# Performance work log

Hardware: AMD Instinct MI355X
Metric: run time of the kernel (lower is better)

## Reference

```python
import jax, jax.numpy as jnp
import numpy as np

N = 20000   # nodes (spots)
E = 100000  # edges (kNN spatial graph, avg degree 5)
IN = 256    # input feature dim = out_dim[-1]
D = 512     # per-head output dim = in_dim (gene count)
H = 4       # heads
NEG_SLOPE = 0.2  # DGL GATv2Conv default negative_slope; fc LeakyReLU slope is also 0.2


def setup_inputs() -> dict:
    key = jax.random.key(0)
    ks = jax.random.split(key, 10)
    s = 0.02
    return {
        "z": jax.random.normal(ks[0], (N, IN), jnp.float32),
        "src": jax.random.randint(ks[1], (E,), 0, N, jnp.int32),
        "dst": jax.random.randint(ks[2], (E,), 0, N, jnp.int32),
        "W_src": jax.random.normal(ks[3], (IN, H * D), jnp.float32) * s,
        "b_src": jnp.zeros((H * D,), jnp.float32),
        "W_dst": jax.random.normal(ks[4], (IN, H * D), jnp.float32) * s,
        "b_dst": jnp.zeros((H * D,), jnp.float32),
        "attn": jax.random.normal(ks[5], (H, D), jnp.float32) * s,
        "gat_bias": jnp.zeros((H * D,), jnp.float32),
        "W_fc": jax.random.normal(ks[6], (H * D, D), jnp.float32) * s,
        "b_fc": jnp.zeros((D,), jnp.float32),
    }


def reference(z, src, dst, W_src, b_src, W_dst, b_dst, attn, gat_bias, W_fc, b_fc):
    # GATv2Conv (DGL semantics, share_weights=False, eval mode so dropout is identity)
    feat_src = (z @ W_src + b_src).reshape(N, H, D)  # [N,H,D]
    feat_dst = (z @ W_dst + b_dst).reshape(N, H, D)  # [N,H,D]
    # per-edge GATv2 score: a^T LeakyReLU(Wsrc h_u + Wdst h_v)
    e = jax.nn.leaky_relu(feat_src[src] + feat_dst[dst], NEG_SLOPE)  # [E,H,D]
    score = jnp.einsum('ehd,hd->eh', e, attn)                        # [E,H]
    # edge softmax over incoming edges of each dst node (numerically stable)
    m = jax.lax.stop_gradient(
        jnp.full((N, H), -jnp.inf, score.dtype).at[dst].max(score))
    ex = jnp.exp(score - m[dst])                                     # [E,H]
    denom = jnp.zeros((N, H), ex.dtype).at[dst].add(ex)              # [N,H]
    alpha = ex / denom[dst]                                          # [E,H]
    # scatter-aggregate messages
    msg = alpha[:, :, None] * feat_src[src]                          # [E,H,D]
    rst = jnp.zeros((N, H, D), msg.dtype).at[dst].add(msg)
    rst = rst + gat_bias.reshape(1, H, D)
    # flatten heads, then fused Linear + LeakyReLU(0.2)
    flat = rst.reshape(N, H * D)
    return jax.nn.leaky_relu(flat @ W_fc + b_fc, NEG_SLOPE)          # [N,D]
```

## Files before the change

kernel.cpp:

```cpp
#include <hip/hip_runtime.h>
#include <hip/hip_bf16.h>
#include <math.h>

#define H_HEADS 4
#define D_HEAD 512
#define HD 2048
#define IN_DIM 256
#define OUTD 512
#define NEG 0.2f

typedef __hip_bfloat16 bf16;
typedef _Float16 f16;
typedef __attribute__((ext_vector_type(2))) _Float16 h2v;
typedef __attribute__((ext_vector_type(8))) short s16x8;
typedef __attribute__((ext_vector_type(4))) float f32x4;

__device__ __forceinline__ float bflo(unsigned w) { union { unsigned u; float f; } x; x.u = w << 16; return x.f; }
__device__ __forceinline__ float bfhi(unsigned w) { union { unsigned u; float f; } x; x.u = w & 0xffff0000u; return x.f; }

template<int MODE>
__global__ __launch_bounds__(256)
void mfma_gemm_kernel(const bf16* __restrict__ A, int lda, long aOff,
                      const bf16* __restrict__ Bt, int ldb, long bOff,
                      const float* __restrict__ bias, long biasOff,
                      const float* __restrict__ bias2, const int* __restrict__ rowptr,
                      void* __restrict__ Cv, int ldc, long cOff,
                      int M, int K)
{
    constexpr int SMEM_BYTES = (MODE == 1) ? (64 * 132 * 4) : (128 * 136 * 2);
    static_assert(SMEM_BYTES >= 4 * 4096 * 2, "staging dbuf must fit");
    __shared__ __align__(16) char smem_raw[SMEM_BYTES];
    bf16* stg = (bf16*)smem_raw;

    const int tid  = threadIdx.x;
    const int r0   = blockIdx.y * 128;
    const int n0   = blockIdx.x * 128;
    const int z    = blockIdx.z;
    const int lane = tid & 63;
    const int wave = tid >> 6;
    const int wr   = (wave >> 1) * 64;
    const int wc   = (wave & 1) * 64;
    const int l15  = lane & 15;
    const int quad = lane >> 4;

    const bf16* Az = A + aOff * (long)z;
    const bf16* Bz = Bt + bOff * (long)z;

    f32x4 acc[4][4];
    #pragma unroll
    for (int i = 0; i < 4; i++)
        #pragma unroll
        for (int j = 0; j < 4; j++)
            #pragma unroll
            for (int r = 0; r < 4; r++) acc[i][j][r] = 0.f;

    const int srow = tid >> 2;
    const int skof = (((tid & 3) ^ ((srow >> 1) & 3)) * 8);
    const int swz  = (l15 >> 1) & 3;

    auto stage_tile = [&](int c, int k0) {
        bf16* As = stg + c * 8192;
        bf16* Bs = As + 4096;
        #pragma unroll
        for (int p = 0; p < 2; p++) {
            int ar = r0 + p * 64 + srow;
            if (ar >= M) ar = M - 1;
            const bf16* ga = Az + (size_t)ar * lda + k0 + skof;
            __builtin_amdgcn_global_load_lds(
                (const __attribute__((address_space(1))) void*)ga,
                (__attribute__((address_space(3))) void*)(As + (p * 256 + tid) * 8),
                16, 0, 0);
            const bf16* gb = Bz + (size_t)(n0 + p * 64 + srow) * ldb + k0 + skof;
            __builtin_amdgcn_global_load_lds(
                (const __attribute__((address_space(1))) void*)gb,
                (__attribute__((address_space(3))) void*)(Bs + (p * 256 + tid) * 8),
                16, 0, 0);
        }
    };

    stage_tile(0, 0);
    int cbuf = 0;
    for (int k0 = 0; k0 < K; k0 += 32) {
        __syncthreads();
        if (k0 + 32 < K) stage_tile(cbuf ^ 1, k0 + 32);

        const bf16* As = stg + cbuf * 8192;
        const bf16* Bs = As + 4096;
        s16x8 af[4], bg[4];
        #pragma unroll
        for (int i = 0; i < 4; i++)
            af[i] = *(const s16x8*)(As + (wr + i * 16 + l15) * 32 + (quad ^ swz) * 8);
        #pragma unroll
        for (int j = 0; j < 4; j++)
            bg[j] = *(const s16x8*)(Bs + (wc + j * 16 + l15) * 32 + (quad ^ swz) * 8);
        #pragma unroll
        for (int i = 0; i < 4; i++)
            #pragma unroll
            for (int j = 0; j < 4; j++)
                acc[i][j] = __builtin_amdgcn_mfma_f32_16x16x32_bf16(af[i], bg[j], acc[i][j], 0, 0, 0);
        cbuf ^= 1;
    }
    __syncthreads();

    if (MODE == 0 || MODE == 2) {
        float bv[4];
        #pragma unroll
        for (int j = 0; j < 4; j++)
            bv[j] = bias ? bias[biasOff * (long)z + n0 + wc + j * 16 + l15] : 0.f;

        const long cb = cOff * (long)z;

        if (MODE == 0) {
            bf16* Cs = (bf16*)smem_raw;
            #pragma unroll
            for (int i = 0; i < 4; i++)
                #pragma unroll
                for (int j = 0; j < 4; j++)
                    #pragma unroll
                    for (int r = 0; r < 4; r++)
                        Cs[(wr + i * 16 + quad * 4 + r) * 136 + wc + j * 16 + l15] =
                            __float2bfloat16(acc[i][j][r] + bv[j]);
        } else {
            f16* Cs = (f16*)smem_raw;
            #pragma unroll
            for (int i = 0; i < 4; i++)
                #pragma unroll
                for (int j = 0; j < 4; j++)
                    #pragma unroll
                    for (int r = 0; r < 4; r++)
                        Cs[(wr + i * 16 + quad * 4 + r) * 136 + wc + j * 16 + l15] =
                            (f16)(acc[i][j][r] + bv[j]);
        }
        __syncthreads();
        #pragma unroll
        for (int it = 0; it < 8; it++) {
            const int idx  = it * 256 + tid;
            const int lrow = idx >> 4;
            const int lcol = (idx & 15) * 8;
            const int grow = r0 + lrow;
            if (grow < M)
                *(uint4*)((short*)Cv + cb + (size_t)grow * ldc + n0 + lcol) =
                    *(const uint4*)((const short*)smem_raw + lrow * 136 + lcol);
        }
    } else {
        float* C = (float*)Cv;
        float* Csf = (float*)smem_raw;

        #pragma unroll
        for (int p = 0; p < 2; p++) {
            __syncthreads();
            if (wr == p * 64) {
                #pragma unroll
                for (int i = 0; i < 4; i++)
                    #pragma unroll
                    for (int j = 0; j < 4; j++)
                        #pragma unroll
                        for (int r = 0; r < 4; r++)
                            Csf[(i * 16 + quad * 4 + r) * 132 + wc + j * 16 + l15] = acc[i][j][r];
            }
            __syncthreads();
            #pragma unroll
            for (int it = 0; it < 8; it++) {
                const int idx  = it * 256 + tid;
                const int lrow = idx >> 5;
                const int lcol = (idx & 31) * 4;
                const int grow = r0 + p * 64 + lrow;
                if (grow < M) {
                    const int gcol = n0 + lcol;
                    float4 v  = *(const float4*)(Csf + lrow * 132 + lcol);
                    const float4 c4 = *(const float4*)(bias + gcol);
                    const float4 b4 = *(const float4*)(bias2 + gcol);
                    const bool has = rowptr[grow + 1] > rowptr[grow];
                    v.x += c4.x + (has ? b4.x : 0.f);
                    v.y += c4.y + (has ? b4.y : 0.f);
                    v.z += c4.z + (has ? b4.z : 0.f);
                    v.w += c4.w + (has ? b4.w : 0.f);
                    v.x = v.x > 0.f ? v.x : NEG * v.x;
                    v.y = v.y > 0.f ? v.y : NEG * v.y;
                    v.z = v.z > 0.f ? v.z : NEG * v.z;
                    v.w = v.w > 0.f ? v.w : NEG * v.w;
                    *(float4*)(C + (size_t)grow * ldc + gcol) = v;
                }
            }
        }
    }
}

__global__ __launch_bounds__(256)
void prep_kernel(const float* __restrict__ W_src, const float* __restrict__ W_dst,
                 const float* __restrict__ W_fc, const float* __restrict__ b_src,
                 const float* __restrict__ b_dst, const float* __restrict__ attn,
                 const float* __restrict__ b_fc, const float* __restrict__ gat_bias,
                 bf16* __restrict__ WsbT, bf16* __restrict__ WdbT,
                 bf16* __restrict__ WfcT, bf16* __restrict__ Wsb,
                 float* __restrict__ bias_cat, f16* __restrict__ atn16,
                 int* __restrict__ cnt, int nCnt,
                 float* __restrict__ cvec, float* __restrict__ bsW_tot, int prepBlocks)
{
    __shared__ float red[256];
    if ((int)blockIdx.x >= prepBlocks) {
        const int b = blockIdx.x - prepBlocks;
        const int t = threadIdx.x;
        const bool isCvec = b < OUTD;
        const int j = isCvec ? b : b - OUTD;
        const float* vec = isCvec ? gat_bias : b_src;
        float s = 0.f;
        for (int k = t; k < HD; k += 256)
            s = fmaf(vec[k], W_fc[(size_t)k * OUTD + j], s);
        red[t] = s;
        __syncthreads();
        for (int o = 128; o > 0; o >>= 1) {
            if (t < o) red[t] += red[t + o];
            __syncthreads();
        }
        if (t == 0) {
            if (isCvec) cvec[j] = red[0] + b_fc[j];
            else bsW_tot[j] = red[0];
        }
        return;
    }
    int idx = blockIdx.x * 256 + threadIdx.x;
    if (idx < 524288) {
        const int n = idx >> 8, k = idx & 255;
        WsbT[idx] = __float2bfloat16(W_src[(size_t)k * HD + n]);
        return;
    }
    idx -= 524288;
    if (idx < 524288) {
        const int n = idx >> 8, k = idx & 255;
        WdbT[idx] = __float2bfloat16(W_dst[(size_t)k * HD + n]);
        return;
    }
    idx -= 524288;
    if (idx < 1048576) {
        const int n = idx >> 9, t = idx & 511;
        const int h = n >> 9, j = n & 511;
        WfcT[idx] = __float2bfloat16(W_fc[(size_t)(h * 512 + t) * OUTD + j]);
        return;
    }
    idx -= 1048576;
    if (idx < 524288) {
        Wsb[idx] = __float2bfloat16(W_src[idx]);
        return;
    }
    idx -= 524288;
    if (idx < 2 * HD) {
        bias_cat[idx] = (idx < HD) ? b_src[idx] : b_dst[idx - HD];
        return;
    }
    idx -= 2 * HD;
    if (idx < HD) {
        atn16[idx] = (f16)attn[idx];
        return;
    }
    idx -= HD;
    if (idx < nCnt) cnt[idx] = 0;
}

__global__ void cast_hist_kernel(const float* __restrict__ S, bf16* __restrict__ T,
                                 long n4, const int* __restrict__ dst,
                                 int* __restrict__ cnt, int E)
{
    long t = (long)blockIdx.x * 256 + threadIdx.x;
    if (t < n4) {
        const long i = t * 4;
        const float4 v = *(const float4*)(S + i);
        T[i + 0] = __float2bfloat16(v.x);
        T[i + 1] = __float2bfloat16(v.y);
        T[i + 2] = __float2bfloat16(v.z);
        T[i + 3] = __float2bfloat16(v.w);
        return;
    }
    t -= n4;
    if (t < E) atomicAdd(&cnt[dst[t]], 1);
}

__global__ __launch_bounds__(1024)
void scan_kernel(const int* __restrict__ cnt, int* __restrict__ rowptr,
                 int* __restrict__ cursor, int n)
{
    __shared__ int wsum[16];
    __shared__ int carry_s;
    const int tid  = threadIdx.x;
    const int lane = tid & 63;
    const int wv   = tid >> 6;
    if (tid == 0) { carry_s = 0; rowptr[0] = 0; cursor[0] = 0; }
    __syncthreads();
    for (int base = 0; base < n; base += 1024) {
        const int i = base + tid;
        int v = (i < n) ? cnt[i] : 0;
        #pragma unroll
        for (int d = 1; d < 64; d <<= 1) {
            const int t = __shfl_up(v, d, 64);
            if (lane >= d) v += t;
        }
        if (lane == 63) wsum[wv] = v;
        __syncthreads();
        if (tid < 16) {
            int w = wsum[tid];
            #pragma unroll
            for (int d = 1; d < 16; d <<= 1) {
                const int t = __shfl_up(w, d, 64);
                if (tid >= d) w += t;
            }
            wsum[tid] = w;
        }
        __syncthreads();
        const int incl = v + (wv ? wsum[wv - 1] : 0) + carry_s;
        if (i < n) {
            rowptr[i + 1] = incl;
            if (i + 1 < n) cursor[i + 1] = incl;
        }
        __syncthreads();
        if (tid == 1023) carry_s += wsum[15];
        __syncthreads();
    }
}

__global__ void scatter_kernel(const int* __restrict__ src, const int* __restrict__ dst,
                               int* __restrict__ cursor, int* __restrict__ csr_src, int E)
{
    const int e = blockIdx.x * 256 + threadIdx.x;
    if (e >= E) return;
    const int pos = atomicAdd(&cursor[dst[e]], 1);
    csr_src[pos] = src[e];
}

__device__ __forceinline__ float score_head_h2(const uint4 pa, const uint4 pb, const uint4 at)
{
    const unsigned* ua = (const unsigned*)&pa;
    const unsigned* ub = (const unsigned*)&pb;
    const unsigned* ut = (const unsigned*)&at;
    h2v acc = (h2v)(_Float16)0.f;
    const h2v c06 = (h2v)(_Float16)0.6f;
    const h2v c04 = (h2v)(_Float16)0.4f;
    #pragma unroll
    for (int c = 0; c < 4; c++) {
        union { unsigned u; h2v h; } A, B, T, S, Ab;
        A.u = ua[c]; B.u = ub[c]; T.u = ut[c];
        S.h = A.h + B.h;
        Ab.u = S.u & 0x7fff7fffu;
        const h2v l = S.h * c06 + Ab.h * c04;
        acc += l * T.h;
    }
    return (float)acc.x + (float)acc.y;
}

__global__ __launch_bounds__(256)
void score_agg_kernel(const f16* __restrict__ fs, const f16* __restrict__ fd,
                      const bf16* __restrict__ zb,
                      const int* __restrict__ rowptr, const int* __restrict__ csr_src,
                      const f16* __restrict__ atn16, bf16* __restrict__ agg, int N)
{
    const int h    = threadIdx.x >> 6;
    const int lane = threadIdx.x & 63;
    const int v    = blockIdx.x;
    if (v >= N) return;

    const uint4 at = *(const uint4*)(atn16 + h * D_HEAD + lane * 8);
    const f16* fsh = fs + h * D_HEAD + (size_t)lane * 8;

    const int off0 = rowptr[v], off1 = rowptr[v + 1];
    const int deg  = off1 - off0;
    float acc[4] = {0.f, 0.f, 0.f, 0.f};
    float den = 0.f;

    const uint4 fdr = *(const uint4*)(fd + (size_t)v * HD + h * D_HEAD + lane * 8);

    for (int e = 0; e < deg; e += 4) {
        const int i0 = off0 + e;
        const int i1 = off0 + ((e + 1 < deg) ? e + 1 : e);
        const int i2 = off0 + ((e + 2 < deg) ? e + 2 : e);
        const int i3 = off0 + ((e + 3 < deg) ? e + 3 : e);
        const int u0 = csr_src[i0], u1 = csr_src[i1], u2 = csr_src[i2], u3 = csr_src[i3];

        const uint4 pa0 = *(const uint4*)(fsh + (size_t)u0 * HD);
        const uint4 pa1 = *(const uint4*)(fsh + (size_t)u1 * HD);
        const uint4 pa2 = *(const uint4*)(fsh + (size_t)u2 * HD);
        const uint4 pa3 = *(const uint4*)(fsh + (size_t)u3 * HD);
        const uint2 z0 = *(const uint2*)(zb + (size_t)u0 * IN_DIM + lane * 4);
        const uint2 z1 = *(const uint2*)(zb + (size_t)u1 * IN_DIM + lane * 4);
        const uint2 z2 = *(const uint2*)(zb + (size_t)u2 * IN_DIM + lane * 4);
        const uint2 z3 = *(const uint2*)(zb + (size_t)u3 * IN_DIM + lane * 4);

        float s0 = score_head_h2(pa0, fdr, at);
        float s1 = score_head_h2(pa1, fdr, at);
        float s2 = score_head_h2(pa2, fdr, at);
        float s3 = score_head_h2(pa3, fdr, at);
        #pragma unroll
        for (int ofs = 32; ofs > 0; ofs >>= 1) {
            s0 += __shfl_xor(s0, ofs, 64);
            s1 += __shfl_xor(s1, ofs, 64);
            s2 += __shfl_xor(s2, ofs, 64);
            s3 += __shfl_xor(s3, ofs, 64);
        }
        const float e0 = __expf(s0);
        const float e1 = (e + 1 < deg) ? __expf(s1) : 0.f;
        const float e2 = (e + 2 < deg) ? __expf(s2) : 0.f;
        const float e3 = (e + 3 < deg) ? __expf(s3) : 0.f;
        den += e0 + e1 + e2 + e3;
        const float zc0[4] = {bflo(z0.x), bfhi(z0.x), bflo(z0.y), bfhi(z0.y)};
        const float zc1[4] = {bflo(z1.x), bfhi(z1.x), bflo(z1.y), bfhi(z1.y)};
        const float zc2[4] = {bflo(z2.x), bfhi(z2.x), bflo(z2.y), bfhi(z2.y)};
        const float zc3[4] = {bflo(z3.x), bfhi(z3.x), bflo(z3.y), bfhi(z3.y)};
        #pragma unroll
        for (int c = 0; c < 4; c++)
            acc[c] += (e0 * zc0[c] + e1 * zc1[c]) + (e2 * zc2[c] + e3 * zc3[c]);
    }
    if (deg > 0) {
        const float inv = 1.f / den;
        #pragma unroll
        for (int c = 0; c < 4; c++) acc[c] *= inv;
    }

    union { uint2 u; short s[4]; } pk;
    #pragma unroll
    for (int c = 0; c < 4; c++) {
        const bf16 b = __float2bfloat16(acc[c]);
        pk.s[c] = *(const short*)&b;
    }
    *(uint2*)(agg + (size_t)v * (H_HEADS * IN_DIM) + h * IN_DIM + lane * 4) = pk.u;
}

__global__ __launch_bounds__(256)
void score_csr_kernel(const f16* __restrict__ fs, const f16* __restrict__ fd,
                      const int* __restrict__ rowptr, const int* __restrict__ csr_src,
                      const f16* __restrict__ atn16, float* __restrict__ expbuf,
                      float* __restrict__ denomB, int N)
{
    const int wave = threadIdx.x >> 6;
    const int lane = threadIdx.x & 63;
    const int wgid = blockIdx.x * 4 + wave;
    const int nw   = gridDim.x * 4;

    uint4 at[H_HEADS];
    #pragma unroll
    for (int h = 0; h < H_HEADS; h++)
        at[h] = *(const uint4*)(atn16 + h * D_HEAD + lane * 8);

    for (int v = wgid; v < N; v += nw) {
        const int off0 = rowptr[v], off1 = rowptr[v + 1];
        if (off0 == off1) continue;
        uint4 fdr[H_HEADS];
        #pragma unroll
        for (int h = 0; h < H_HEADS; h++)
            fdr[h] = *(const uint4*)(fd + (size_t)v * HD + h * D_HEAD + lane * 8);

        float4 den = make_float4(0.f, 0.f, 0.f, 0.f);
        for (int o = off0; o < off1; o += 2) {
            const bool two = (o + 1 < off1);
            const int u0 = csr_src[o];
            const int u1 = two ? csr_src[o + 1] : u0;
            const f16* f0 = fs + (size_t)u0 * HD + lane * 8;
            const f16* f1 = fs + (size_t)u1 * HD + lane * 8;
            uint4 pa0[H_HEADS], pa1[H_HEADS];
            #pragma unroll
            for (int h = 0; h < H_HEADS; h++) pa0[h] = *(const uint4*)(f0 + h * D_HEAD);
            #pragma unroll
            for (int h = 0; h < H_HEADS; h++) pa1[h] = *(const uint4*)(f1 + h * D_HEAD);

            float s0[H_HEADS], s1[H_HEADS];
            #pragma unroll
            for (int h = 0; h < H_HEADS; h++) {
                s0[h] = score_head_h2(pa0[h], fdr[h], at[h]);
                s1[h] = score_head_h2(pa1[h], fdr[h], at[h]);
            }
            #pragma unroll
            for (int ofs = 32; ofs > 0; ofs >>= 1) {
                #pragma unroll
                for (int h = 0; h < H_HEADS; h++) {
                    s0[h] += __shfl_xor(s0[h], ofs, 64);
                    s1[h] += __shfl_xor(s1[h], ofs, 64);
                }
            }
            const float4 e0 = make_float4(expf(s0[0]), expf(s0[1]), expf(s0[2]), expf(s0[3]));
            den.x += e0.x; den.y += e0.y; den.z += e0.z; den.w += e0.w;
            float4 e1;
            if (two) {
                e1 = make_float4(expf(s1[0]), expf(s1[1]), expf(s1[2]), expf(s1[3]));
                den.x += e1.x; den.y += e1.y; den.z += e1.z; den.w += e1.w;
            }
            if (lane == 0) {
                *(float4*)(expbuf + (size_t)o * H_HEADS) = e0;
                if (two) *(float4*)(expbuf + (size_t)(o + 1) * H_HEADS) = e1;
            }
        }
        if (lane == 0) *(float4*)(denomB + (size_t)v * H_HEADS) = den;
    }
}

__global__ __launch_bounds__(256)
void agg_z_kernel(const bf16* __restrict__ zb, const int* __restrict__ rowptr,
                  const int* __restrict__ csr_src, const float* __restrict__ expbuf,
                  const float* __restrict__ denomB, bf16* __restrict__ agg, int N)
{
    const int wave = threadIdx.x >> 6;
    const int lane = threadIdx.x & 63;
    const int wgid = blockIdx.x * 4 + wave;
    const int nw   = gridDim.x * 4;

    for (int v = wgid; v < N; v += nw) {
        const int off0 = rowptr[v], off1 = rowptr[v + 1];
        float acc[H_HEADS][4];
        #pragma unroll
        for (int h = 0; h < H_HEADS; h++)
            #pragma unroll
            for (int c = 0; c < 4; c++) acc[h][c] = 0.f;

        if (off1 > off0) {
            const float4 den = *(const float4*)(denomB + (size_t)v * H_HEADS);
            const float4 inv = make_float4(1.f / den.x, 1.f / den.y, 1.f / den.z, 1.f / den.w);
            int o = off0;
            for (; o + 1 < off1; o += 2) {
                const float4 e0 = *(const float4*)(expbuf + (size_t)o * H_HEADS);
                const float4 e1 = *(const float4*)(expbuf + (size_t)(o + 1) * H_HEADS);
                const int u0 = csr_src[o], u1 = csr_src[o + 1];
                const uint2 z0 = *(const uint2*)(zb + (size_t)u0 * IN_DIM + lane * 4);
                const uint2 z1 = *(const uint2*)(zb + (size_t)u1 * IN_DIM + lane * 4);
                const float a0[4] = {e0.x * inv.x, e0.y * inv.y, e0.z * inv.z, e0.w * inv.w};
                const float a1[4] = {e1.x * inv.x, e1.y * inv.y, e1.z * inv.z, e1.w * inv.w};
                const float zc0[4] = {bflo(z0.x), bfhi(z0.x), bflo(z0.y), bfhi(z0.y)};
                const float zc1[4] = {bflo(z1.x), bfhi(z1.x), bflo(z1.y), bfhi(z1.y)};
                #pragma unroll
                for (int h = 0; h < H_HEADS; h++)
                    #pragma unroll
                    for (int c = 0; c < 4; c++)
                        acc[h][c] += a0[h] * zc0[c] + a1[h] * zc1[c];
            }
            if (o < off1) {
                const float4 e0 = *(const float4*)(expbuf + (size_t)o * H_HEADS);
                const int u0 = csr_src[o];
                const uint2 z0 = *(const uint2*)(zb + (size_t)u0 * IN_DIM + lane * 4);
                const float a0[4] = {e0.x * inv.x, e0.y * inv.y, e0.z * inv.z, e0.w * inv.w};
                const float zc0[4] = {bflo(z0.x), bfhi(z0.x), bflo(z0.y), bfhi(z0.y)};
                #pragma unroll
                for (int h = 0; h < H_HEADS; h++)
                    #pragma unroll
                    for (int c = 0; c < 4; c++)
                        acc[h][c] += a0[h] * zc0[c];
            }
        }
        #pragma unroll
        for (int h = 0; h < H_HEADS; h++) {
            union { uint2 u; short s[4]; } pk;
            #pragma unroll
            for (int c = 0; c < 4; c++) {
                const bf16 b = __float2bfloat16(acc[h][c]);
                pk.s[c] = *(const short*)&b;
            }
            *(uint2*)(agg + (size_t)v * (H_HEADS * IN_DIM) + h * IN_DIM + lane * 4) = pk.u;
        }
    }
}

extern "C" void kernel_launch(void* const* d_in, const int* in_sizes, int n_in,
                              void* d_out, int out_size, void* d_ws, size_t ws_size,
                              hipStream_t stream)
{
    const float* z        = (const float*)d_in[0];
    const int*   src      = (const int*)d_in[1];
    const int*   dst      = (const int*)d_in[2];
    const float* W_src    = (const float*)d_in[3];
    const float* b_src    = (const float*)d_in[4];
    const float* W_dst    = (const float*)d_in[5];
    const float* b_dst    = (const float*)d_in[6];
    const float* attn     = (const float*)d_in[7];
    const float* gat_bias = (const float*)d_in[8];
    const float* W_fc     = (const float*)d_in[9];
    const float* b_fc     = (const float*)d_in[10];
    float* out = (float*)d_out;

    const int N = in_sizes[0] / IN_DIM;
    const int E = in_sizes[1];

    char* p = (char*)d_ws;
    const size_t featB = (size_t)N * HD * 2;
    f16* fs       = (f16*)p;   p += featB;
    f16* fd       = (f16*)p;   p += featB;
    bf16* zb      = (bf16*)p;  p += (size_t)N * IN_DIM * sizeof(bf16);
    bf16* WsbT    = (bf16*)p;  p += (size_t)HD * IN_DIM * sizeof(bf16);
    bf16* WdbT    = (bf16*)p;  p += (size_t)HD * IN_DIM * sizeof(bf16);
    bf16* Wsb     = (bf16*)p;  p += (size_t)IN_DIM * HD * sizeof(bf16);
    bf16* WfcT    = (bf16*)p;  p += (size_t)HD * D_HEAD * sizeof(bf16);
    bf16* Wfinal  = (bf16*)p;  p += (size_t)OUTD * 1024 * sizeof(bf16);
    float* bias_cat = (float*)p; p += (size_t)2 * HD * sizeof(float);
    f16* atn16    = (f16*)p;   p += (size_t)HD * sizeof(f16);
    float* bsW_tot = (float*)p; p += (size_t)OUTD * sizeof(float);
    float* cvec   = (float*)p; p += (size_t)OUTD * sizeof(float);
    float* expbuf = (float*)p; p += (size_t)E * H_HEADS * sizeof(float);
    float* denomB = (float*)p; p += (size_t)N * H_HEADS * sizeof(float);
    int* cnt      = (int*)p;   p += ((size_t)N * 4 + 15) & ~15ULL;
    int* rowptr   = (int*)p;   p += ((size_t)(N + 1) * 4 + 15) & ~15ULL;
    int* cursor   = (int*)p;   p += ((size_t)N * 4 + 15) & ~15ULL;
    int* csr_src  = (int*)p;   p += ((size_t)E * 4 + 15) & ~15ULL;

    bf16* aggSep = (bf16*)p;
    const size_t needFused = (size_t)(p - (char*)d_ws) + (size_t)N * (H_HEADS * IN_DIM) * sizeof(bf16);
    const bool fused = (ws_size >= needFused);
    bf16* agg = fused ? aggSep : (bf16*)fs;

    const int prepElems  = 524288 * 3 + 1048576 + 2 * HD + HD + N;
    const int prepBlocks = (prepElems + 255) / 256;
    prep_kernel<<<prepBlocks + 2 * OUTD, 256, 0, stream>>>(
        W_src, W_dst, W_fc, b_src, b_dst, attn, b_fc, gat_bias,
        WsbT, WdbT, WfcT, Wsb, bias_cat, atn16, cnt, N, cvec, bsW_tot, prepBlocks);

    const long n4 = (long)N * IN_DIM / 4;
    cast_hist_kernel<<<(int)((n4 + E + 255) / 256), 256, 0, stream>>>(z, zb, n4, dst, cnt, E);

    scan_kernel<<<1, 1024, 0, stream>>>(cnt, rowptr, cursor, N);
    scatter_kernel<<<(E + 255) / 256, 256, 0, stream>>>(src, dst, cursor, csr_src, E);

    mfma_gemm_kernel<0><<<dim3(IN_DIM / 128, D_HEAD / 128, H_HEADS), 256, 0, stream>>>(
        WfcT, D_HEAD, (long)D_HEAD * D_HEAD,
        Wsb, HD, (long)D_HEAD,
        nullptr, 0, nullptr, nullptr,
        Wfinal, 1024, (long)IN_DIM,
        D_HEAD, D_HEAD);

    mfma_gemm_kernel<2><<<dim3(HD / 128, (N + 127) / 128, 2), 256, 0, stream>>>(
        zb, IN_DIM, 0L,
        WsbT, IN_DIM, (long)HD * IN_DIM,
        bias_cat, (long)HD, nullptr, nullptr,
        fs, HD, (long)N * HD,
        N, IN_DIM);

    if (fused) {
        score_agg_kernel<<<N, 256, 0, stream>>>(fs, fd, zb, rowptr, csr_src, atn16, agg, N);
    } else {
        score_csr_kernel<<<2500, 256, 0, stream>>>(fs, fd, rowptr, csr_src, atn16, expbuf, denomB, N);
        agg_z_kernel<<<2500, 256, 0, stream>>>(zb, rowptr, csr_src, expbuf, denomB, agg, N);
    }

    mfma_gemm_kernel<1><<<dim3(OUTD / 128, (N + 127) / 128, 1), 256, 0, stream>>>(
        agg, H_HEADS * IN_DIM, 0L,
        Wfinal, H_HEADS * IN_DIM, 0L,
        cvec, 0L, bsW_tot, rowptr,
        out, OUTD, 0L,
        N, H_HEADS * IN_DIM);
}
```

Measured before the change: 357.4 us.

## Tile weight transposes through shared memory and parallelize CSR prefix scan

The prep kernel now transposes W_src, W_dst and W_fc through 32x33 shared-memory tiles, so both the reads and the writes are coalesced instead of strided gathers. Wsb casting is vectorized with float4 loads. The single-block serial scan over 20000 counts is replaced by a two-pass multi-block scan: local block scans, then a per-block offset computed from the block sums. This adds one kernel launch and caps the scan at 128 blocks, about 32K nodes.

```diff
diff --git a/kernel.cpp b/kernel.cpp
--- a/kernel.cpp
+++ b/kernel.cpp
@@ -195,66 +195,90 @@
                  bf16* __restrict__ WfcT, bf16* __restrict__ Wsb,
                  float* __restrict__ bias_cat, f16* __restrict__ atn16,
                  int* __restrict__ cnt, int nCnt,
-                 float* __restrict__ cvec, float* __restrict__ bsW_tot, int prepBlocks)
-{
-    __shared__ float red[256];
-    if ((int)blockIdx.x >= prepBlocks) {
-        const int b = blockIdx.x - prepBlocks;
-        const int t = threadIdx.x;
-        const bool isCvec = b < OUTD;
-        const int j = isCvec ? b : b - OUTD;
+                 float* __restrict__ cvec, float* __restrict__ bsW_tot, int miscB)
+{
+    __shared__ float tile[32][33];
+    const int b   = blockIdx.x;
+    const int tid = threadIdx.x;
+    const int tx  = tid & 31;
+    const int ty0 = tid >> 5;
+
+    if (b < 1024) {
+        const float* In = (b < 512) ? W_src : W_dst;
+        bf16* Out       = (b < 512) ? WsbT : WdbT;
+        const int a  = b & 511;
+        const int bk = a & 7;
+        const int bn = a >> 3;
+        #pragma unroll
+        for (int i = 0; i < 4; i++) {
+            const int r = ty0 + i * 8;
+            tile[r][tx] = In[(size_t)(bk * 32 + r) * HD + bn * 32 + tx];
+        }
+        __syncthreads();
+        #pragma unroll
+        for (int i = 0; i < 4; i++) {
+            const int r = ty0 + i * 8;
+            Out[(size_t)(bn * 32 + r) * IN_DIM + bk * 32 + tx] = __float2bfloat16(tile[tx][r]);
+        }
+        return;
+    }
+    if (b < 2048) {
+        const int c  = b - 1024;
+        const int h  = c >> 8;
+        const int r8 = c & 255;
+        const int bt = r8 & 15;
+        const int bj = r8 >> 4;
+        #pragma unroll
+        for (int i = 0; i < 4; i++) {
+            const int r = ty0 + i * 8;
+            tile[r][tx] = W_fc[(size_t)(h * 512 + bt * 32 + r) * OUTD + bj * 32 + tx];
+        }
+        __syncthreads();
+        #pragma unroll
+        for (int i = 0; i < 4; i++) {
+            const int r = ty0 + i * 8;
+            WfcT[(size_t)(h * 512 + bj * 32 + r) * 512 + bt * 32 + tx] = __float2bfloat16(tile[tx][r]);
+        }
+        return;
+    }
+    if (b < 2560) {
+        const int i4 = ((b - 2048) * 256 + tid) * 4;
+        const float4 v = *(const float4*)(W_src + i4);
+        Wsb[i4 + 0] = __float2bfloat16(v.x);
+        Wsb[i4 + 1] = __float2bfloat16(v.y);
+        Wsb[i4 + 2] = __float2bfloat16(v.z);
+        Wsb[i4 + 3] = __float2bfloat16(v.w);
+        return;
+    }
+    if (b < 2560 + miscB) {
+        int idx = (b - 2560) * 256 + tid;
+        if (idx < 2 * HD) { bias_cat[idx] = (idx < HD) ? b_src[idx] : b_dst[idx - HD]; return; }
+        idx -= 2 * HD;
+        if (idx < HD) { atn16[idx] = (f16)attn[idx]; return; }
+        idx -= HD;
+        if (idx < nCnt) cnt[idx] = 0;
+        return;
+    }
+    {
+        __shared__ float red[256];
+        const int rb = b - (2560 + miscB);
+        const bool isCvec = rb < OUTD;
+        const int j = isCvec ? rb : rb - OUTD;
         const float* vec = isCvec ? gat_bias : b_src;
         float s = 0.f;
-        for (int k = t; k < HD; k += 256)
+        for (int k = tid; k < HD; k += 256)
             s = fmaf(vec[k], W_fc[(size_t)k * OUTD + j], s);
-        red[t] = s;
+        red[tid] = s;
         __syncthreads();
         for (int o = 128; o > 0; o >>= 1) {
-            if (t < o) red[t] += red[t + o];
+            if (tid < o) red[tid] += red[tid + o];
             __syncthreads();
         }
-        if (t == 0) {
+        if (tid == 0) {
             if (isCvec) cvec[j] = red[0] + b_fc[j];
             else bsW_tot[j] = red[0];
         }
-        return;
-    }
-    int idx = blockIdx.x * 256 + threadIdx.x;
-    if (idx < 524288) {
-        const int n = idx >> 8, k = idx & 255;
-        WsbT[idx] = __float2bfloat16(W_src[(size_t)k * HD + n]);
-        return;
-    }
-    idx -= 524288;
-    if (idx < 524288) {
-        const int n = idx >> 8, k = idx & 255;
-        WdbT[idx] = __float2bfloat16(W_dst[(size_t)k * HD + n]);
-        return;
-    }
-    idx -= 524288;
-    if (idx < 1048576) {
-        const int n = idx >> 9, t = idx & 511;
-        const int h = n >> 9, j = n & 511;
-        WfcT[idx] = __float2bfloat16(W_fc[(size_t)(h * 512 + t) * OUTD + j]);
-        return;
-    }
-    idx -= 1048576;
-    if (idx < 524288) {
-        Wsb[idx] = __float2bfloat16(W_src[idx]);
-        return;
-    }
-    idx -= 524288;
-    if (idx < 2 * HD) {
-        bias_cat[idx] = (idx < HD) ? b_src[idx] : b_dst[idx - HD];
-        return;
-    }
-    idx -= 2 * HD;
-    if (idx < HD) {
-        atn16[idx] = (f16)attn[idx];
-        return;
-    }
-    idx -= HD;
-    if (idx < nCnt) cnt[idx] = 0;
+    }
 }
 
 __global__ void cast_hist_kernel(const float* __restrict__ S, bf16* __restrict__ T,
@@ -275,46 +299,54 @@
     if (t < E) atomicAdd(&cnt[dst[t]], 1);
 }
 
-__global__ __launch_bounds__(1024)
-void scan_kernel(const int* __restrict__ cnt, int* __restrict__ rowptr,
-                 int* __restrict__ cursor, int n)
-{
-    __shared__ int wsum[16];
-    __shared__ int carry_s;
+__global__ __launch_bounds__(256)
+void scan1_kernel(const int* __restrict__ cnt, int* __restrict__ locIncl,
+                  int* __restrict__ bsum, int n)
+{
+    __shared__ int ws[4];
     const int tid  = threadIdx.x;
     const int lane = tid & 63;
     const int wv   = tid >> 6;
-    if (tid == 0) { carry_s = 0; rowptr[0] = 0; cursor[0] = 0; }
+    const int i    = blockIdx.x * 256 + tid;
+    int v = (i < n) ? cnt[i] : 0;
+    #pragma unroll
+    for (int d = 1; d < 64; d <<= 1) {
+        const int t = __shfl_up(v, d, 64);
+        if (lane >= d) v += t;
+    }
+    if (lane == 63) ws[wv] = v;
     __syncthreads();
-    for (int base = 0; base < n; base += 1024) {
-        const int i = base + tid;
-        int v = (i < n) ? cnt[i] : 0;
-        #pragma unroll
-        for (int d = 1; d < 64; d <<= 1) {
-            const int t = __shfl_up(v, d, 64);
-            if (lane >= d) v += t;
-        }
-        if (lane == 63) wsum[wv] = v;
-        __syncthreads();
-        if (tid < 16) {
-            int w = wsum[tid];
-            #pragma unroll
-            for (int d = 1; d < 16; d <<= 1) {
-                const int t = __shfl_up(w, d, 64);
-                if (tid >= d) w += t;
-            }
-            wsum[tid] = w;
-        }
-        __syncthreads();
-        const int incl = v + (wv ? wsum[wv - 1] : 0) + carry_s;
-        if (i < n) {
-            rowptr[i + 1] = incl;
-            if (i + 1 < n) cursor[i + 1] = incl;
-        }
-        __syncthreads();
-        if (tid == 1023) carry_s += wsum[15];
-        __syncthreads();
-    }
+    int s = 0;
+    if (wv > 0) s += ws[0];
+    if (wv > 1) s += ws[1];
+    if (wv > 2) s += ws[2];
+    const int incl = v + s;
+    locIncl[i] = incl;
+    if (tid == 255) bsum[blockIdx.x] = incl;
+}
+
+__global__ __launch_bounds__(256)
+void scan2_kernel(const int* __restrict__ locIncl, const int* __restrict__ bsum,
+                  int* __restrict__ rowptr, int* __restrict__ cursor, int n, int nb)
+{
+    __shared__ int bs[128];
+    __shared__ int off_s;
+    const int tid = threadIdx.x;
+    if (tid < 128) bs[tid] = (tid < nb) ? bsum[tid] : 0;
+    __syncthreads();
+    if (tid == 0) {
+        int o = 0;
+        for (int w = 0; w < (int)blockIdx.x; w++) o += bs[w];
+        off_s = o;
+    }
+    __syncthreads();
+    const int i = blockIdx.x * 256 + tid;
+    if (i < n) {
+        const int r = locIncl[i] + off_s;
+        rowptr[i + 1] = r;
+        if (i + 1 < n) cursor[i + 1] = r;
+    }
+    if (blockIdx.x == 0 && tid == 0) { rowptr[0] = 0; cursor[0] = 0; }
 }
 
 __global__ void scatter_kernel(const int* __restrict__ src, const int* __restrict__ dst,
@@ -572,6 +604,7 @@
 
     const int N = in_sizes[0] / IN_DIM;
     const int E = in_sizes[1];
+    const int nBlocksScan = (N + 255) / 256;
 
     char* p = (char*)d_ws;
     const size_t featB = (size_t)N * HD * 2;
@@ -593,22 +626,25 @@
     int* rowptr   = (int*)p;   p += ((size_t)(N + 1) * 4 + 15) & ~15ULL;
     int* cursor   = (int*)p;   p += ((size_t)N * 4 + 15) & ~15ULL;
     int* csr_src  = (int*)p;   p += ((size_t)E * 4 + 15) & ~15ULL;
+    int* locIncl  = (int*)p;   p += ((size_t)nBlocksScan * 256 * 4 + 15) & ~15ULL;
+    int* bsum     = (int*)p;   p += ((size_t)128 * 4 + 15) & ~15ULL;
 
     bf16* aggSep = (bf16*)p;
     const size_t needFused = (size_t)(p - (char*)d_ws) + (size_t)N * (H_HEADS * IN_DIM) * sizeof(bf16);
     const bool fused = (ws_size >= needFused);
     bf16* agg = fused ? aggSep : (bf16*)fs;
 
-    const int prepElems  = 524288 * 3 + 1048576 + 2 * HD + HD + N;
-    const int prepBlocks = (prepElems + 255) / 256;
-    prep_kernel<<<prepBlocks + 2 * OUTD, 256, 0, stream>>>(
+    const int miscElems = 2 * HD + HD + N;
+    const int miscB = (miscElems + 255) / 256;
+    prep_kernel<<<2560 + miscB + 2 * OUTD, 256, 0, stream>>>(
         W_src, W_dst, W_fc, b_src, b_dst, attn, b_fc, gat_bias,
-        WsbT, WdbT, WfcT, Wsb, bias_cat, atn16, cnt, N, cvec, bsW_tot, prepBlocks);
+        WsbT, WdbT, WfcT, Wsb, bias_cat, atn16, cnt, N, cvec, bsW_tot, miscB);
 
     const long n4 = (long)N * IN_DIM / 4;
     cast_hist_kernel<<<(int)((n4 + E + 255) / 256), 256, 0, stream>>>(z, zb, n4, dst, cnt, E);
 
-    scan_kernel<<<1, 1024, 0, stream>>>(cnt, rowptr, cursor, N);
+    scan1_kernel<<<nBlocksScan, 256, 0, stream>>>(cnt, locIncl, bsum, N);
+    scan2_kernel<<<nBlocksScan, 256, 0, stream>>>(locIncl, bsum, rowptr, cursor, N, nBlocksScan);
     scatter_kernel<<<(E + 255) / 256, 256, 0, stream>>>(src, dst, cursor, csr_src, E);
 
     mfma_gemm_kernel<0><<<dim3(IN_DIM / 128, D_HEAD / 128, H_HEADS), 256, 0, stream>>>(
```

After: 332.6 us. 1.07x faster.
